# Kernel optimization log

Measured on AMD Instinct MI355X. Metric: run time of the kernel, lower is better.

The kernel has to match this reference:

```python
import jax, jax.numpy as jnp
import numpy as np

N, IN_F, OUT_F, H = 4096, 256, 64, 8


def setup_inputs() -> dict:
    key = jax.random.key(0)
    k1, k2, k3, k4 = jax.random.split(key, 4)
    features = jax.random.normal(k1, (N, IN_F), dtype=jnp.float32)
    adj_matrix = jax.random.randint(k2, (N, N), 0, 2, dtype=jnp.int32)
    # xavier_uniform bounds
    bw = float(np.sqrt(6.0 / (IN_F + OUT_F)))
    W = jax.random.uniform(k3, (IN_F, OUT_F), dtype=jnp.float32, minval=-bw, maxval=bw)
    ba = float(np.sqrt(6.0 / (2 * OUT_F + 1)))
    attention = jax.random.uniform(k4, (H, 2 * OUT_F, 1), dtype=jnp.float32, minval=-ba, maxval=ba)
    return {"features": features, "adj_matrix": adj_matrix, "W": W, "attention": attention}


def reference(features, adj_matrix, W, attention):
    h = features @ W                      # [N, F]
    F = h.shape[1]
    a_src = attention[:, :F, 0]           # [H, F] (dotted with row node h_i)
    a_dst = attention[:, F:, 0]           # [H, F] (dotted with col node h_j)
    # score[h,i,j] = <concat(h_i, h_j), a_h> = src[h,i] + dst[h,j]
    src = jnp.einsum('nf,hf->hn', h, a_src)   # [H, N]
    dst = jnp.einsum('nf,hf->hn', h, a_dst)   # [H, N]
    scores = src[:, :, None] + dst[:, None, :]           # [H, N, N]
    NEG = jnp.float32(-9e15)
    scores = jnp.where(adj_matrix[None, :, :] > 0, scores, NEG)
    alpha = jax.nn.softmax(scores, axis=-1)               # [H, N, N]
    alpha = jnp.mean(alpha, axis=0)                       # [N, N] (mean over heads)
    return alpha @ h                                      # [N, F]
```

## Files before the change

kernel.cpp:

```cpp
#include <hip/hip_runtime.h>
#include <hip/hip_bf16.h>

#define NN   4096
#define INF_ 256
#define OUTF 64
#define NH   8
#define HSTR 72
#define NPAD 576

using bf16x8 = __attribute__((ext_vector_type(8))) short;
using f32x4  = __attribute__((ext_vector_type(4))) float;

__device__ __forceinline__ void gload_lds16(const void* g, void* l) {
  __builtin_amdgcn_global_load_lds((__attribute__((address_space(1))) void*)(g),
                                   (__attribute__((address_space(3))) void*)(l),
                                   16, 0, 0);
}

__device__ __forceinline__ unsigned short f2bf(float x) {
  unsigned u = __float_as_uint(x);
  unsigned r = (u + 0x7FFFu + ((u >> 16) & 1u)) >> 16;
  return (unsigned short)r;
}

__global__ __launch_bounds__(256) void k_prep(const float* __restrict__ feat,
                                              const float* __restrict__ W,
                                              const float* __restrict__ att,
                                              unsigned short* __restrict__ Gt) {
  __shared__ float fl[16][INF_];
  __shared__ float hl[16][65];
  __shared__ float el[NH][16];
  int j0 = blockIdx.x * 16;
  int tid = threadIdx.x;
  const float4* src = (const float4*)(feat + (size_t)j0 * INF_);
  for (int i = tid; i < 16 * 64; i += 256) {
    int r = i >> 6, c4 = i & 63;
    *(float4*)&fl[r][c4 * 4] = src[i];
  }
  __syncthreads();
  int c  = tid & 63;
  int rg = tid >> 6;
  float acc[4] = {0.f, 0.f, 0.f, 0.f};
#pragma unroll 8
  for (int k = 0; k < INF_; ++k) {
    float w = W[k * OUTF + c];
#pragma unroll
    for (int m = 0; m < 4; ++m) acc[m] = fmaf(fl[rg * 4 + m][k], w, acc[m]);
  }
#pragma unroll
  for (int m = 0; m < 4; ++m) hl[rg * 4 + m][c] = acc[m];
  __syncthreads();
  if (tid < NH * 16) {
    int hh = tid >> 4, row = tid & 15;
    float d = 0.f;
#pragma unroll 8
    for (int f = 0; f < 64; ++f) d = fmaf(hl[row][f], att[hh * 128 + 64 + f], d);
    el[hh][row] = expf(d);
  }
  __syncthreads();
  for (int i = tid; i < NPAD * 8; i += 256) {
    int u = i & 7, cc = i >> 3;
    int j2 = u * 2;
    int hh2 = cc / HSTR, c2 = cc - hh2 * HSTR;
    float e0 = el[hh2][j2], e1 = el[hh2][j2 + 1];
    float v0, v1;
    if (c2 < 64)      { v0 = e0 * hl[j2][c2]; v1 = e1 * hl[j2 + 1][c2]; }
    else if (c2 == 64){ v0 = e0;              v1 = e1; }
    else              { v0 = 0.f;             v1 = 0.f; }
    ushort2 o; o.x = f2bf(v0); o.y = f2bf(v1);
    *(ushort2*)&Gt[(size_t)cc * NN + j0 + j2] = o;
  }
}

#define BM 64
#define BN 192
#define BK 64
#define KS 4
#define NT 16
#define NTILE 3
#define MTILE 64
#define BSZ (BN * BK)

#define SEP()      asm volatile("" ::: "memory")
#define WAITVM(N)  asm volatile("s_waitcnt vmcnt(" #N ")" ::: "memory")
#define WAITLGKM() asm volatile("s_waitcnt lgkmcnt(0)" ::: "memory")
#define BAR()      asm volatile("s_barrier" ::: "memory")

__global__ __launch_bounds__(256, 2) void k_gemm(const int* __restrict__ adj,
                                                 const unsigned short* __restrict__ Bsrc,
                                                 float* __restrict__ Cp) {
  __shared__ alignas(16) unsigned short As[BM * BK];
  __shared__ alignas(16) unsigned short Bs[2][BSZ];

  int id  = blockIdx.x;
  int wg  = (id & 7) * (768 >> 3) + (id >> 3);
  int nt  = wg % NTILE;
  int mt  = (wg / NTILE) % MTILE;
  int ks  = wg / (NTILE * MTILE);

  int m0 = mt * BM, n0 = nt * BN, k0 = ks * (NT * BK);
  int tid = threadIdx.x;
  int lane = tid & 63, wid = tid >> 6;
  int wm = wid >> 1, wn = wid & 1;
  f32x4 acc[2][6] = {};

  int srow = tid >> 2;
  int sgrp = tid & 3;
  const int* Ag = adj + (size_t)(m0 + srow) * NN + k0 + sgrp * 8;
  unsigned ad0 = (unsigned)srow * BK + (unsigned)((sgrp    ) ^ (srow & 7)) * 8;
  unsigned ad1 = (unsigned)srow * BK + (unsigned)((sgrp + 4) ^ (srow & 7)) * 8;

  int brow = tid >> 3, bgrp = tid & 7;
  const unsigned short* Bg = Bsrc + (size_t)(n0 + brow) * NN + k0
                           + (size_t)((bgrp ^ (brow & 7)) * 8);

  int4 ra[4];

#define ALOAD(KO)                                                             \
  do {                                                                        \
    const int4* p = (const int4*)(Ag + (KO));                                 \
    ra[0] = p[0]; ra[1] = p[1];                                               \
    const int4* q = (const int4*)(Ag + (KO) + 32);                            \
    ra[2] = q[0]; ra[3] = q[1];                                               \
  } while (0)

#define AWRITE()                                                              \
  do {                                                                        \
    unsigned w0 = (unsigned)(ra[0].x | (ra[0].y << 16)) * 0x3F80u;            \
    unsigned w1 = (unsigned)(ra[0].z | (ra[0].w << 16)) * 0x3F80u;            \
    unsigned w2 = (unsigned)(ra[1].x | (ra[1].y << 16)) * 0x3F80u;            \
    unsigned w3 = (unsigned)(ra[1].z | (ra[1].w << 16)) * 0x3F80u;            \
    *(uint4*)&As[ad0] = make_uint4(w0, w1, w2, w3);                           \
    unsigned v0 = (unsigned)(ra[2].x | (ra[2].y << 16)) * 0x3F80u;            \
    unsigned v1 = (unsigned)(ra[2].z | (ra[2].w << 16)) * 0x3F80u;            \
    unsigned v2 = (unsigned)(ra[3].x | (ra[3].y << 16)) * 0x3F80u;            \
    unsigned v3 = (unsigned)(ra[3].z | (ra[3].w << 16)) * 0x3F80u;            \
    *(uint4*)&As[ad1] = make_uint4(v0, v1, v2, v3);                           \
  } while (0)

#define BSTAGE(BB, KO)                                                        \
  do { _Pragma("unroll") for (int r = 0; r < 6; ++r)                          \
    gload_lds16(Bg + (size_t)(r * 32) * NN + (KO),                            \
                &Bs[BB][(unsigned)((r * 32 + wid * 8) * BK)]);                \
  } while (0)

  int hi = lane >> 4, r15 = lane & 15, x7 = lane & 7;

#define COMPUTE(BB)                                                           \
  do { _Pragma("unroll") for (int kk = 0; kk < 2; ++kk) {                     \
    bf16x8 af[2], bfr[6];                                                     \
    _Pragma("unroll") for (int m = 0; m < 2; ++m)                             \
      af[m] = *(const bf16x8*)&As[(wm * 32 + m * 16 + r15) * BK +             \
                                  (((kk * 4 + hi) ^ x7) * 8)];                \
    _Pragma("unroll") for (int n = 0; n < 6; ++n)                             \
      bfr[n] = *(const bf16x8*)&Bs[BB][(wn * 96 + n * 16 + r15) * BK +        \
                                       (((kk * 4 + hi) ^ x7) * 8)];           \
    _Pragma("unroll") for (int m = 0; m < 2; ++m)                             \
      _Pragma("unroll") for (int n = 0; n < 6; ++n)                           \
        acc[m][n] = __builtin_amdgcn_mfma_f32_16x16x32_bf16(af[m], bfr[n],    \
                                                            acc[m][n], 0,0,0);\
  } } while (0)

  ALOAD(0); SEP(); BSTAGE(0, 0); SEP();

  for (int kt = 0; kt < NT; ++kt) {
    int cur = kt & 1;
    WAITVM(6);
    WAITLGKM();
    BAR();
    AWRITE();
    if (kt + 1 < NT) {
      int ko = (kt + 1) * BK;
      ALOAD(ko); SEP();
      BSTAGE(cur ^ 1, ko);
      WAITVM(10);
    } else {
      WAITVM(0);
    }
    WAITLGKM();
    BAR();
    COMPUTE(cur);
  }

  float* Cout = Cp + (size_t)ks * NN * NPAD;
#pragma unroll
  for (int m = 0; m < 2; ++m)
#pragma unroll
    for (int n = 0; n < 6; ++n)
#pragma unroll
      for (int j = 0; j < 4; ++j) {
        int row = m0 + wm * 32 + m * 16 + hi * 4 + j;
        int col = n0 + wn * 96 + n * 16 + r15;
        Cout[(size_t)row * NPAD + col] = acc[m][n][j];
      }
#undef ALOAD
#undef AWRITE
#undef BSTAGE
#undef COMPUTE
}

__global__ __launch_bounds__(256) void k_epi(const float* __restrict__ Cp,
                                             float* __restrict__ out) {
  int idx = blockIdx.x * 256 + threadIdx.x;
  int i = idx >> 6, f = idx & 63;
  const float* row = Cp + (size_t)i * NPAD;
  const size_t stride = (size_t)NN * NPAD;
  float s = 0.f;
#pragma unroll
  for (int hh = 0; hh < NH; ++hh) {
    float num = 0.f, den = 0.f;
#pragma unroll
    for (int ks = 0; ks < KS; ++ks) {
      num += row[ks * stride + hh * HSTR + f];
      den += row[ks * stride + hh * HSTR + 64];
    }
    float inv = (den > 0.f) ? (1.f / den) : 0.f;
    s = fmaf(num, inv, s);
  }
  out[idx] = 0.125f * s;
}

extern "C" void kernel_launch(void* const* d_in, const int* in_sizes, int n_in,
                              void* d_out, int out_size, void* d_ws, size_t ws_size,
                              hipStream_t stream) {
  const float* feat = (const float*)d_in[0];
  const int*   adj  = (const int*)d_in[1];
  const float* W    = (const float*)d_in[2];
  const float* att  = (const float*)d_in[3];
  float* out = (float*)d_out;

  const size_t GT_B = (size_t)NPAD * NN * 2;
  char* ws = (char*)d_ws;
  unsigned short* Gt = (unsigned short*)(ws);
  float*          Cp = (float*)(ws + GT_B);

  k_prep<<<NN / 16, 256, 0, stream>>>(feat, W, att, Gt);
  k_gemm<<<NTILE * MTILE * KS, 256, 0, stream>>>(adj, Gt, Cp);
  k_epi <<<NN * OUTF / 256, 256, 0, stream>>>(Cp, out);
}
```

Before: 66.39 us.

## Deepen GEMM prefetch to two stages with triple-buffered B tiles

Replaces the double-buffered B tile in LDS with a triple buffer. It also adds two register sets for prefetching the adjacency (A) tile, so loads for k-tile t+2 are in flight while tile t is computed. The A load mapping changes to 32 rows per thread group with a second row 32 below, and the vmcnt waits are retuned for the deeper queue. This aims to hide more global-memory latency, at the cost of more VGPRs and more LDS per block (about 80KB), which may limit occupancy. Several dead AWRITE macro drafts remain but are undefined before use.

```diff
diff --git a/kernel.cpp b/kernel.cpp
--- a/kernel.cpp
+++ b/kernel.cpp
@@ -90,7 +90,7 @@
                                                  const unsigned short* __restrict__ Bsrc,
                                                  float* __restrict__ Cp) {
   __shared__ alignas(16) unsigned short As[BM * BK];
-  __shared__ alignas(16) unsigned short Bs[2][BSZ];
+  __shared__ alignas(16) unsigned short Bs[3 * BSZ];
 
   int id  = blockIdx.x;
   int wg  = (id & 7) * (768 >> 3) + (id >> 3);
@@ -104,83 +104,154 @@
   int wm = wid >> 1, wn = wid & 1;
   f32x4 acc[2][6] = {};
 
-  int srow = tid >> 2;
-  int sgrp = tid & 3;
-  const int* Ag = adj + (size_t)(m0 + srow) * NN + k0 + sgrp * 8;
-  unsigned ad0 = (unsigned)srow * BK + (unsigned)((sgrp    ) ^ (srow & 7)) * 8;
-  unsigned ad1 = (unsigned)srow * BK + (unsigned)((sgrp + 4) ^ (srow & 7)) * 8;
-
-  int brow = tid >> 3, bgrp = tid & 7;
-  const unsigned short* Bg = Bsrc + (size_t)(n0 + brow) * NN + k0
-                           + (size_t)((bgrp ^ (brow & 7)) * 8);
-
-  int4 ra[4];
-
-#define ALOAD(KO)                                                             \
-  do {                                                                        \
-    const int4* p = (const int4*)(Ag + (KO));                                 \
-    ra[0] = p[0]; ra[1] = p[1];                                               \
-    const int4* q = (const int4*)(Ag + (KO) + 32);                            \
-    ra[2] = q[0]; ra[3] = q[1];                                               \
-  } while (0)
-
-#define AWRITE()                                                              \
-  do {                                                                        \
-    unsigned w0 = (unsigned)(ra[0].x | (ra[0].y << 16)) * 0x3F80u;            \
-    unsigned w1 = (unsigned)(ra[0].z | (ra[0].w << 16)) * 0x3F80u;            \
-    unsigned w2 = (unsigned)(ra[1].x | (ra[1].y << 16)) * 0x3F80u;            \
-    unsigned w3 = (unsigned)(ra[1].z | (ra[1].w << 16)) * 0x3F80u;            \
-    *(uint4*)&As[ad0] = make_uint4(w0, w1, w2, w3);                           \
-    unsigned v0 = (unsigned)(ra[2].x | (ra[2].y << 16)) * 0x3F80u;            \
-    unsigned v1 = (unsigned)(ra[2].z | (ra[2].w << 16)) * 0x3F80u;            \
-    unsigned v2 = (unsigned)(ra[3].x | (ra[3].y << 16)) * 0x3F80u;            \
-    unsigned v3 = (unsigned)(ra[3].z | (ra[3].w << 16)) * 0x3F80u;            \
-    *(uint4*)&As[ad1] = make_uint4(v0, v1, v2, v3);                           \
-  } while (0)
-
-#define BSTAGE(BB, KO)                                                        \
+  int arow = tid >> 3;
+  int agrp = tid & 7;
+  int aswz = agrp ^ (arow & 7);
+  const int* Ag = adj + (size_t)(m0 + arow) * NN + k0 + agrp * 8;
+  unsigned ad0 = (unsigned)arow * BK + (unsigned)aswz * 8;
+  unsigned ad1 = (unsigned)(arow + 32) * BK + (unsigned)aswz * 8;
+
+  const unsigned short* Bg = Bsrc + (size_t)(n0 + arow) * NN + k0
+                           + (size_t)(aswz * 8);
+
+  int4 ra0[2], ra1[2];
+
+#define ALOAD(RA, KO)                                                         \
+  do {                                                                        \
+    RA[0] = *(const int4*)(Ag + (KO));                                        \
+    RA[1] = *(const int4*)(Ag + (size_t)32 * NN + (KO));                      \
+  } while (0)
+
+#define AWRITE(RA)                                                            \
+  do {                                                                        \
+    unsigned w0 = (unsigned)(RA[0].x | (RA[0].y << 16)) * 0x3F80u;            \
+    unsigned w1 = (unsigned)(RA[0].z | (RA[0].w << 16)) * 0x3F80u;            \
+    unsigned w2 = (unsigned)(RA[1].x | (RA[1].y << 16)) * 0x3F80u;            \
+    unsigned w3 = (unsigned)(RA[1].z | (RA[1].w << 16)) * 0x3F80u;            \
+    *(uint4*)&As[ad0] = make_uint4(w0, w1, (unsigned)(RA[0].x ^ RA[0].x), 0); \
+  } while (0)
+#undef AWRITE
+#define AWRITE(RA)                                                            \
+  do {                                                                        \
+    unsigned w0 = (unsigned)(RA[0].x | (RA[0].y << 16)) * 0x3F80u;            \
+    unsigned w1 = (unsigned)(RA[0].z | (RA[0].w << 16)) * 0x3F80u;            \
+    unsigned w2 = (unsigned)(RA[0].z, 0u);                                    \
+  } while (0)
+#undef AWRITE
+#define AWRITE(RA)                                                            \
+  do {                                                                        \
+    unsigned a0 = (unsigned)(RA[0].x | (RA[0].y << 16)) * 0x3F80u;            \
+    unsigned a1 = (unsigned)(RA[0].z | (RA[0].w << 16)) * 0x3F80u;            \
+    const int4* hp = &RA[0];                                                  \
+    unsigned a2 = (unsigned)(hp[0].x, 0u); (void)a2;                          \
+  } while (0)
+#undef AWRITE
+#define AWRITE(RA)                                                            \
+  do {                                                                        \
+    unsigned p0 = (unsigned)(RA[0].x | (RA[0].y << 16)) * 0x3F80u;            \
+    unsigned p1 = (unsigned)(RA[0].z | (RA[0].w << 16)) * 0x3F80u;            \
+    int4 lo2 = RA[1];                                                         \
+    unsigned p2 = (unsigned)(lo2.x | (lo2.y << 16)) * 0x3F80u;                \
+    unsigned p3 = (unsigned)(lo2.z | (lo2.w << 16)) * 0x3F80u;                \
+    *(uint2*)&As[ad0]     = make_uint2(p0, p1);                               \
+    *(uint2*)&As[ad0 + 4] = make_uint2(0, 0);                                 \
+  } while (0)
+#undef AWRITE
+#define AWRITE(RA)                                                            \
+  do {                                                                        \
+    unsigned q0 = (unsigned)(RA[0].x | (RA[0].y << 16)) * 0x3F80u;            \
+    unsigned q1 = (unsigned)(RA[0].z | (RA[0].w << 16)) * 0x3F80u;            \
+    unsigned q2 = (unsigned)(RA[1].x | (RA[1].y << 16)) * 0x3F80u;            \
+    unsigned q3 = (unsigned)(RA[1].z | (RA[1].w << 16)) * 0x3F80u;            \
+    *(uint4*)&As[ad0] = make_uint4(q0, q1, 0u, 0u);                           \
+    *(uint4*)&As[ad1] = make_uint4(q2, q3, 0u, 0u);                           \
+  } while (0)
+#undef AWRITE
+#define AWRITE(RA)                                                            \
+  do {                                                                        \
+    unsigned s0 = (unsigned)(RA[0].x | (RA[0].y << 16)) * 0x3F80u;            \
+    unsigned s1 = (unsigned)(RA[0].z | (RA[0].w << 16)) * 0x3F80u;            \
+    unsigned s2 = (unsigned)(RA[1].x | (RA[1].y << 16)) * 0x3F80u;            \
+    unsigned s3 = (unsigned)(RA[1].z | (RA[1].w << 16)) * 0x3F80u;            \
+    *(uint2*)&As[ad0] = make_uint2(s0, s1);                                   \
+    *(uint2*)&As[ad1] = make_uint2(s2, s3);                                   \
+  } while (0)
+#undef ALOAD
+#undef AWRITE
+
+  int4 rb0[4], rb1[4];
+
+#define ALOAD2(RA, KO)                                                        \
+  do {                                                                        \
+    const int4* p0_ = (const int4*)(Ag + (KO));                               \
+    RA[0] = p0_[0]; RA[1] = p0_[1];                                           \
+    const int4* p1_ = (const int4*)(Ag + (size_t)32 * NN + (KO));             \
+    RA[2] = p1_[0]; RA[3] = p1_[1];                                           \
+  } while (0)
+
+#define AWRITE2(RA)                                                           \
+  do {                                                                        \
+    unsigned t0 = (unsigned)(RA[0].x | (RA[0].y << 16)) * 0x3F80u;            \
+    unsigned t1 = (unsigned)(RA[0].z | (RA[0].w << 16)) * 0x3F80u;            \
+    unsigned t2 = (unsigned)(RA[1].x | (RA[1].y << 16)) * 0x3F80u;            \
+    unsigned t3 = (unsigned)(RA[1].z | (RA[1].w << 16)) * 0x3F80u;            \
+    *(uint4*)&As[ad0] = make_uint4(t0, t1, t2, t3);                           \
+    unsigned u0 = (unsigned)(RA[2].x | (RA[2].y << 16)) * 0x3F80u;            \
+    unsigned u1 = (unsigned)(RA[2].z | (RA[2].w << 16)) * 0x3F80u;            \
+    unsigned u2 = (unsigned)(RA[3].x | (RA[3].y << 16)) * 0x3F80u;            \
+    unsigned u3 = (unsigned)(RA[3].z | (RA[3].w << 16)) * 0x3F80u;            \
+    *(uint4*)&As[ad1] = make_uint4(u0, u1, u2, u3);                           \
+  } while (0)
+
+#define BSTAGE(BIO, KO)                                                       \
   do { _Pragma("unroll") for (int r = 0; r < 6; ++r)                          \
     gload_lds16(Bg + (size_t)(r * 32) * NN + (KO),                            \
-                &Bs[BB][(unsigned)((r * 32 + wid * 8) * BK)]);                \
+                &Bs[(unsigned)(BIO) + (unsigned)((r * 32 + wid * 8) * BK)]);  \
   } while (0)
 
   int hi = lane >> 4, r15 = lane & 15, x7 = lane & 7;
 
-#define COMPUTE(BB)                                                           \
+#define COMPUTE(BCO)                                                          \
   do { _Pragma("unroll") for (int kk = 0; kk < 2; ++kk) {                     \
     bf16x8 af[2], bfr[6];                                                     \
     _Pragma("unroll") for (int m = 0; m < 2; ++m)                             \
       af[m] = *(const bf16x8*)&As[(wm * 32 + m * 16 + r15) * BK +             \
                                   (((kk * 4 + hi) ^ x7) * 8)];                \
     _Pragma("unroll") for (int n = 0; n < 6; ++n)                             \
-      bfr[n] = *(const bf16x8*)&Bs[BB][(wn * 96 + n * 16 + r15) * BK +        \
-                                       (((kk * 4 + hi) ^ x7) * 8)];           \
+      bfr[n] = *(const bf16x8*)&Bs[(unsigned)(BCO) +                          \
+                                   (unsigned)((wn * 96 + n * 16 + r15) * BK) \
+                                   + (unsigned)(((kk * 4 + hi) ^ x7) * 8)];   \
     _Pragma("unroll") for (int m = 0; m < 2; ++m)                             \
       _Pragma("unroll") for (int n = 0; n < 6; ++n)                           \
         acc[m][n] = __builtin_amdgcn_mfma_f32_16x16x32_bf16(af[m], bfr[n],    \
                                                             acc[m][n], 0,0,0);\
   } } while (0)
 
-  ALOAD(0); SEP(); BSTAGE(0, 0); SEP();
-
-  for (int kt = 0; kt < NT; ++kt) {
-    int cur = kt & 1;
-    WAITVM(6);
-    WAITLGKM();
-    BAR();
-    AWRITE();
-    if (kt + 1 < NT) {
-      int ko = (kt + 1) * BK;
-      ALOAD(ko); SEP();
-      BSTAGE(cur ^ 1, ko);
-      WAITVM(10);
-    } else {
-      WAITVM(0);
-    }
-    WAITLGKM();
-    BAR();
-    COMPUTE(cur);
-  }
+#define GITER(RA, WA, DOI, WB)                                                \
+  WA;                                                                         \
+  WAITLGKM();                                                                 \
+  BAR();                                                                      \
+  AWRITE2(RA);                                                                \
+  if (DOI) { ALOAD2(RA, koff); SEP(); BSTAGE(bio, koff); koff += BK; }        \
+  WB;                                                                         \
+  WAITLGKM();                                                                 \
+  BAR();                                                                      \
+  COMPUTE(bco);                                                               \
+  bco += BSZ; if (bco == 3 * BSZ) bco = 0;                                    \
+  bio += BSZ; if (bio == 3 * BSZ) bio = 0;
+
+  ALOAD2(rb0, 0);  SEP();  BSTAGE(0, 0);    SEP();
+  ALOAD2(rb1, BK); SEP();  BSTAGE(BSZ, BK); SEP();
+
+  int bco = 0, bio = 2 * BSZ;
+  int koff = 2 * BK;
+
+  for (int k2 = 0; k2 < 7; ++k2) {
+    GITER(rb0, WAITVM(16), 1, WAITVM(20));
+    GITER(rb1, WAITVM(16), 1, WAITVM(20));
+  }
+  GITER(rb0, WAITVM(16), 0, WAITVM(10));
+  GITER(rb1, WAITVM(6), 0, WAITVM(0));
 
   float* Cout = Cp + (size_t)ks * NN * NPAD;
 #pragma unroll
@@ -193,10 +264,11 @@
         int col = n0 + wn * 96 + n * 16 + r15;
         Cout[(size_t)row * NPAD + col] = acc[m][n][j];
       }
-#undef ALOAD
-#undef AWRITE
+#undef ALOAD2
+#undef AWRITE2
 #undef BSTAGE
 #undef COMPUTE
+#undef GITER
 }
 
 __global__ __launch_bounds__(256) void k_epi(const float* __restrict__ Cp,
```

New measurement: 65.06 us. -2.0%, faster.

## Load adjacency fragments directly into registers and triple-buffer B tiles

Applied to the files above, without the earlier changes.

The GEMM tile changes from 64x192 to 128x96, with each warp owning 32 rows across the full N width. The adjacency operand now goes straight from global memory into MFMA A-fragments through inline dwordx4 loads, skipping the LDS staging store and reload. B tiles use a three-slot LDS ring prefetched two steps ahead, so each iteration needs only one barrier, and occupancy is raised to 3 blocks per SM. The aims are less LDS traffic, fewer barriers and deeper overlap of loads with compute. The trade-off is higher register pressure, and the hand-counted vmcnt waits are fragile.

```diff
diff --git a/kernel.cpp b/kernel.cpp
--- a/kernel.cpp
+++ b/kernel.cpp
@@ -10,11 +10,18 @@
 
 using bf16x8 = __attribute__((ext_vector_type(8))) short;
 using f32x4  = __attribute__((ext_vector_type(4))) float;
+using i32x4  = __attribute__((ext_vector_type(4))) int;
 
 __device__ __forceinline__ void gload_lds16(const void* g, void* l) {
   __builtin_amdgcn_global_load_lds((__attribute__((address_space(1))) void*)(g),
                                    (__attribute__((address_space(3))) void*)(l),
                                    16, 0, 0);
+}
+
+__device__ __forceinline__ i32x4 gload_i4(const int* p) {
+  i32x4 r;
+  asm volatile("global_load_dwordx4 %0, %1, off" : "=v"(r) : "v"(p));
+  return r;
 }
 
 __device__ __forceinline__ unsigned short f2bf(float x) {
@@ -72,25 +79,25 @@
   }
 }
 
-#define BM 64
-#define BN 192
+#define BM 128
+#define BN 96
 #define BK 64
 #define KS 4
 #define NT 16
-#define NTILE 3
-#define MTILE 64
+#define NTILE 6
+#define MTILE 32
 #define BSZ (BN * BK)
 
 #define SEP()      asm volatile("" ::: "memory")
 #define WAITVM(N)  asm volatile("s_waitcnt vmcnt(" #N ")" ::: "memory")
 #define WAITLGKM() asm volatile("s_waitcnt lgkmcnt(0)" ::: "memory")
 #define BAR()      asm volatile("s_barrier" ::: "memory")
-
-__global__ __launch_bounds__(256, 2) void k_gemm(const int* __restrict__ adj,
+#define SCHEDBAR() __builtin_amdgcn_sched_barrier(0)
+
+__global__ __launch_bounds__(256, 3) void k_gemm(const int* __restrict__ adj,
                                                  const unsigned short* __restrict__ Bsrc,
                                                  float* __restrict__ Cp) {
-  __shared__ alignas(16) unsigned short As[BM * BK];
-  __shared__ alignas(16) unsigned short Bs[2][BSZ];
+  __shared__ alignas(16) unsigned short Bs[3 * BSZ];
 
   int id  = blockIdx.x;
   int wg  = (id & 7) * (768 >> 3) + (id >> 3);
@@ -101,85 +108,79 @@
   int m0 = mt * BM, n0 = nt * BN, k0 = ks * (NT * BK);
   int tid = threadIdx.x;
   int lane = tid & 63, wid = tid >> 6;
-  int wm = wid >> 1, wn = wid & 1;
   f32x4 acc[2][6] = {};
 
-  int srow = tid >> 2;
-  int sgrp = tid & 3;
-  const int* Ag = adj + (size_t)(m0 + srow) * NN + k0 + sgrp * 8;
-  unsigned ad0 = (unsigned)srow * BK + (unsigned)((sgrp    ) ^ (srow & 7)) * 8;
-  unsigned ad1 = (unsigned)srow * BK + (unsigned)((sgrp + 4) ^ (srow & 7)) * 8;
+  int hi = lane >> 4, r15 = lane & 15, x7 = lane & 7;
+
+  const int* A0 = adj + (size_t)(m0 + wid * 32 + r15) * NN + k0 + hi * 8;
+  const int* A1 = A0 + (size_t)16 * NN;
 
   int brow = tid >> 3, bgrp = tid & 7;
   const unsigned short* Bg = Bsrc + (size_t)(n0 + brow) * NN + k0
                            + (size_t)((bgrp ^ (brow & 7)) * 8);
 
-  int4 ra[4];
+  i32x4 ra[2][2][2];
 
 #define ALOAD(KO)                                                             \
   do {                                                                        \
-    const int4* p = (const int4*)(Ag + (KO));                                 \
-    ra[0] = p[0]; ra[1] = p[1];                                               \
-    const int4* q = (const int4*)(Ag + (KO) + 32);                            \
-    ra[2] = q[0]; ra[3] = q[1];                                               \
+    ra[0][0][0] = gload_i4(A0 + (KO));                                        \
+    ra[0][0][1] = gload_i4(A0 + (KO) + 4);                                    \
+    ra[0][1][0] = gload_i4(A0 + (KO) + 32);                                   \
+    ra[0][1][1] = gload_i4(A0 + (KO) + 36);                                   \
+    ra[1][0][0] = gload_i4(A1 + (KO));                                        \
+    ra[1][0][1] = gload_i4(A1 + (KO) + 4);                                    \
+    ra[1][1][0] = gload_i4(A1 + (KO) + 32);                                   \
+    ra[1][1][1] = gload_i4(A1 + (KO) + 36);                                   \
   } while (0)
 
-#define AWRITE()                                                              \
-  do {                                                                        \
-    unsigned w0 = (unsigned)(ra[0].x | (ra[0].y << 16)) * 0x3F80u;            \
-    unsigned w1 = (unsigned)(ra[0].z | (ra[0].w << 16)) * 0x3F80u;            \
-    unsigned w2 = (unsigned)(ra[1].x | (ra[1].y << 16)) * 0x3F80u;            \
-    unsigned w3 = (unsigned)(ra[1].z | (ra[1].w << 16)) * 0x3F80u;            \
-    *(uint4*)&As[ad0] = make_uint4(w0, w1, w2, w3);                           \
-    unsigned v0 = (unsigned)(ra[2].x | (ra[2].y << 16)) * 0x3F80u;            \
-    unsigned v1 = (unsigned)(ra[2].z | (ra[2].w << 16)) * 0x3F80u;            \
-    unsigned v2 = (unsigned)(ra[3].x | (ra[3].y << 16)) * 0x3F80u;            \
-    unsigned v3 = (unsigned)(ra[3].z | (ra[3].w << 16)) * 0x3F80u;            \
-    *(uint4*)&As[ad1] = make_uint4(v0, v1, v2, v3);                           \
+#define CONVERT()                                                             \
+  do { _Pragma("unroll") for (int m = 0; m < 2; ++m)                          \
+       _Pragma("unroll") for (int kk = 0; kk < 2; ++kk) {                     \
+    i32x4 p = ra[m][kk][0], q = ra[m][kk][1];                                 \
+    union { uint4 u; bf16x8 v; } cv;                                          \
+    cv.u.x = (unsigned)(p[0] | (p[1] << 16)) * 0x3F80u;                       \
+    cv.u.y = (unsigned)(p[2] | (p[3] << 16)) * 0x3F80u;                       \
+    cv.u.z = (unsigned)(q[0] | (q[1] << 16)) * 0x3F80u;                       \
+    cv.u.w = (unsigned)(q[2] | (q[3] << 16)) * 0x3F80u;                       \
+    af[m][kk] = cv.v;                                                         \
+  } } while (0)
+
+#define BSTAGE(BIO, KO)                                                       \
+  do { _Pragma("unroll") for (int r = 0; r < 3; ++r)                          \
+    gload_lds16(Bg + (size_t)(r * 32) * NN + (KO),                            \
+                &Bs[(unsigned)(BIO) + (unsigned)((r * 32 + wid * 8) * BK)]);  \
   } while (0)
 
-#define BSTAGE(BB, KO)                                                        \
-  do { _Pragma("unroll") for (int r = 0; r < 6; ++r)                          \
-    gload_lds16(Bg + (size_t)(r * 32) * NN + (KO),                            \
-                &Bs[BB][(unsigned)((r * 32 + wid * 8) * BK)]);                \
-  } while (0)
-
-  int hi = lane >> 4, r15 = lane & 15, x7 = lane & 7;
-
-#define COMPUTE(BB)                                                           \
+#define COMPUTE(BCO)                                                          \
   do { _Pragma("unroll") for (int kk = 0; kk < 2; ++kk) {                     \
-    bf16x8 af[2], bfr[6];                                                     \
-    _Pragma("unroll") for (int m = 0; m < 2; ++m)                             \
-      af[m] = *(const bf16x8*)&As[(wm * 32 + m * 16 + r15) * BK +             \
-                                  (((kk * 4 + hi) ^ x7) * 8)];                \
+    bf16x8 bfr[6];                                                            \
     _Pragma("unroll") for (int n = 0; n < 6; ++n)                             \
-      bfr[n] = *(const bf16x8*)&Bs[BB][(wn * 96 + n * 16 + r15) * BK +        \
-                                       (((kk * 4 + hi) ^ x7) * 8)];           \
+      bfr[n] = *(const bf16x8*)&Bs[(unsigned)(BCO) +                          \
+                                   (unsigned)((n * 16 + r15) * BK)            \
+                                   + (unsigned)(((kk * 4 + hi) ^ x7) * 8)];   \
     _Pragma("unroll") for (int m = 0; m < 2; ++m)                             \
       _Pragma("unroll") for (int n = 0; n < 6; ++n)                           \
-        acc[m][n] = __builtin_amdgcn_mfma_f32_16x16x32_bf16(af[m], bfr[n],    \
+        acc[m][n] = __builtin_amdgcn_mfma_f32_16x16x32_bf16(af[m][kk], bfr[n],\
                                                             acc[m][n], 0,0,0);\
   } } while (0)
 
-  ALOAD(0); SEP(); BSTAGE(0, 0); SEP();
-
+  bf16x8 af[2][2];
+
+  BSTAGE(0, 0); SEP();
+  ALOAD(0);     SEP();
+  BSTAGE(BSZ, BK);
+
+#pragma unroll
   for (int kt = 0; kt < NT; ++kt) {
-    int cur = kt & 1;
-    WAITVM(6);
+    if (kt < NT - 1) { WAITVM(3); } else { WAITVM(0); }
+    SCHEDBAR();
+    CONVERT();
+    SCHEDBAR();
+    if (kt + 1 < NT) { ALOAD((kt + 1) * BK); SEP(); }
     WAITLGKM();
     BAR();
-    AWRITE();
-    if (kt + 1 < NT) {
-      int ko = (kt + 1) * BK;
-      ALOAD(ko); SEP();
-      BSTAGE(cur ^ 1, ko);
-      WAITVM(10);
-    } else {
-      WAITVM(0);
-    }
-    WAITLGKM();
-    BAR();
-    COMPUTE(cur);
+    if (kt + 2 < NT) BSTAGE((unsigned)(((kt + 2) % 3) * BSZ), (kt + 2) * BK);
+    COMPUTE((unsigned)((kt % 3) * BSZ));
   }
 
   float* Cout = Cp + (size_t)ks * NN * NPAD;
@@ -189,12 +190,12 @@
     for (int n = 0; n < 6; ++n)
 #pragma unroll
       for (int j = 0; j < 4; ++j) {
-        int row = m0 + wm * 32 + m * 16 + hi * 4 + j;
-        int col = n0 + wn * 96 + n * 16 + r15;
+        int row = m0 + wid * 32 + m * 16 + hi * 4 + j;
+        int col = n0 + n * 16 + r15;
         Cout[(size_t)row * NPAD + col] = acc[m][n][j];
       }
 #undef ALOAD
-#undef AWRITE
+#undef CONVERT
 #undef BSTAGE
 #undef COMPUTE
 }
```

Measured after the change: 79.60 us. 1.2x slower.
